# Optimization experiments

Hardware: AMD Instinct MI355X
Metric: run time of the kernel (lower is better)

## Reference

```python
import jax, jax.numpy as jnp
import numpy as np

B, C, T, N = 8, 128, 12, 4096
E_HALF = 131072
EPS = 1e-5


def _linear_params(key, fan_in, fan_out):
    kw, kb = jax.random.split(key)
    bound = 1.0 / np.sqrt(fan_in)
    W = jax.random.uniform(kw, (fan_in, fan_out), jnp.float32, -bound, bound)
    b = jax.random.uniform(kb, (fan_out,), jnp.float32, -bound, bound)
    return W, b


def setup_inputs() -> dict:
    key = jax.random.key(0)
    ks = jax.random.split(key, 10)
    h_in = jax.random.normal(ks[0], (B, C, T, N), jnp.float32)
    # symmetric edge list: random pairs + reverses + self loops
    u = jax.random.randint(ks[1], (E_HALF,), 0, N, jnp.int32)
    v = jax.random.randint(ks[2], (E_HALF,), 0, N, jnp.int32)
    loops = jnp.arange(N, dtype=jnp.int32)
    row = jnp.concatenate([u, v, loops])
    col = jnp.concatenate([v, u, loops])
    edge_index = jnp.stack([row, col])  # [2, E]
    Wq, bq = _linear_params(ks[3], C, C)
    Wk, bk = _linear_params(ks[4], C, C)
    Wv, bv = _linear_params(ks[5], C, C)
    W1, b1 = _linear_params(ks[6], 2 * C, 4 * C)
    W2, b2 = _linear_params(ks[7], 4 * C, C)
    W3, b3 = _linear_params(ks[8], C, 1)
    return dict(h_in=h_in, edge_index=edge_index, Wq=Wq, bq=bq, Wk=Wk, bk=bk,
                Wv=Wv, bv=bv, W1=W1, b1=b1, W2=W2, b2=b2, W3=W3, b3=b3)


def _masked_instance_norm(x, mask_f):
    # stats over the non-self-loop edges only (matching torch, where the MLP
    # only sees edge_index[:, non_self_loop_mask])
    cnt = mask_f.sum()
    mean = (x * mask_f).sum(0) / cnt
    var = (((x - mean) ** 2) * mask_f).sum(0) / cnt
    return (x - mean) / jnp.sqrt(var + EPS)


def _forward(h_in, edge_index, Wq, bq, Wk, bk, Wv, bv, W1, b1, W2, b2, W3, b3):
    # ---- TemporalAttention ----
    x = jnp.transpose(h_in, (0, 3, 2, 1))  # [B, N, T, C]
    q = x @ Wq + bq
    k = x @ Wk + bk
    v = x @ Wv + bv
    scores = jnp.einsum('bntc,bnsc->bnts', q, k) / (C ** 0.5)
    attn = jax.nn.softmax(scores, axis=-1)
    weighted = jnp.einsum('bnts,bnsc->bntc', attn, v)
    emb = weighted.sum(axis=2)          # [B, N, C]
    emb_mean = emb.mean(axis=0)         # [N, C]

    # ---- ExtractorMLP on non-self-loop edges ----
    row, col = edge_index[0], edge_index[1]
    self_loop = row == col
    mask_f = (~self_loop).astype(emb_mean.dtype)[:, None]  # [E, 1]
    f12 = jnp.concatenate([emb_mean[row], emb_mean[col]], axis=-1)  # [E, 2C]
    h = jax.nn.relu(_masked_instance_norm(f12 @ W1 + b1, mask_f))
    h = jax.nn.relu(_masked_instance_norm(h @ W2 + b2, mask_f))
    logits = h @ W3 + b3                 # [E, 1]

    # concrete_sample, eval mode (deterministic)
    att = jax.nn.sigmoid(logits)
    all_att = jnp.where(self_loop[:, None], 1.0, att)  # [E, 1]

    # ---- transpose + reorder_like: match each edge with its reverse ----
    M = jnp.max(edge_index) + 1
    fwd_key = row * M + col
    rev_key = col * M + row
    order = jnp.argsort(fwd_key)
    pos = jnp.searchsorted(fwd_key[order], rev_key)
    perm = order[pos]                    # index of reverse edge
    edge_att = (all_att + all_att[perm]) * 0.5
    return edge_att


def reference(h_in, edge_index, Wq, bq, Wk, bk, Wv, bv, W1, b1, W2, b2, W3, b3):
    return _forward(h_in, edge_index, Wq, bq, Wk, bk, Wv, bv, W1, b1, W2, b2, W3, b3)
```

## Files before the change

kernel.cpp:

```cpp
#include <hip/hip_runtime.h>
#include <hip/hip_bf16.h>

#define CC     128
#define TT     12
#define NNODE  4096
#define NE     266240
#define EHALF  131072
#define F1     512
#define EPS    1e-5f
#define RSQRTC 0.08838834764831845f
#define EB     64
#define NBLKG  4160
#define NF2A   65
#define ST     40

#define O_XWM   0ull
#define O_W1S   524288ull
#define O_W2S   524800ull
#define O_ICNT  525312ull
#define O_CNT   525440ull
#define O_T     529536ull
#define O_S     529664ull
#define O_GTB   546048ull
#define O_W0B   554240ull
#define O_WC1   554304ull
#define O_WC2   619840ull
#define O_B1C   685376ull
#define O_M1    685888ull
#define O_IS1   686400ull
#define O_M2    686912ull
#define O_IS2   687040ull
#define O_CROSS 687168ull
#define O_W2T   687680ull
#define O_PB    720448ull
#define O_QB    1769024ull
#define O_ALLA  2817600ull
#define O_PART  3083840ull
#define O_PART2 4148800ull
#define O_Z2    4165440ull

typedef __attribute__((ext_vector_type(8))) short bf16x8;
typedef __attribute__((ext_vector_type(4))) float f32x4;

__device__ inline float bfbits2f(unsigned int v) { return __uint_as_float(v << 16); }
__device__ inline unsigned short f2bf(float x) {
  union { __hip_bfloat16 h; unsigned short u; } cv;
  cv.h = __float2bfloat16(x);
  return cv.u;
}
__device__ inline float f4get(const float4& v, int k) {
  return k == 0 ? v.x : k == 1 ? v.y : k == 2 ? v.z : v.w;
}

__global__ void k_pre(const float* __restrict__ Wq, const float* __restrict__ bq,
                      const float* __restrict__ Wk,
                      unsigned short* __restrict__ Gtb, unsigned short* __restrict__ w0b) {
  int i = blockIdx.x, j = threadIdx.x;
  float acc = 0.f;
  for (int co = 0; co < CC; ++co) acc = fmaf(Wq[i*CC+co], Wk[j*CC+co], acc);
  Gtb[j*CC + i] = f2bf(acc);
  if (j == 0) {
    float a = 0.f;
    for (int co = 0; co < CC; ++co) a = fmaf(Wk[i*CC+co], bq[co], a);
    w0b[i] = f2bf(a);
  }
}

__global__ __launch_bounds__(256) void k_prew(const float* __restrict__ Wv,
    const float* __restrict__ bv, const float* __restrict__ W1, const float* __restrict__ b1,
    float* __restrict__ Wc1, float* __restrict__ Wc2, float* __restrict__ b1c) {
  __shared__ float wvr[CC];
  const int c = blockIdx.x, tid = threadIdx.x;
  if (tid < CC) wvr[tid] = Wv[(size_t)c*CC + tid];
  __syncthreads();
  for (int h = 0; h < 2; ++h) {
    int f = h*256 + tid;
    float a1 = 0.f, a2 = 0.f;
    for (int j = 0; j < CC; ++j) {
      float wv = wvr[j];
      a1 = fmaf(wv, W1[(size_t)j*F1 + f], a1);
      a2 = fmaf(wv, W1[(size_t)(CC + j)*F1 + f], a2);
    }
    Wc1[(size_t)c*F1 + f] = a1;
    Wc2[(size_t)c*F1 + f] = a2;
  }
  if (c == 0) {
    for (int h = 0; h < 2; ++h) {
      int f = h*256 + tid;
      float s = b1[f];
      for (int j = 0; j < CC; ++j)
        s = fmaf(12.f*bv[j], W1[(size_t)j*F1 + f] + W1[(size_t)(CC + j)*F1 + f], s);
      b1c[f] = s;
    }
  }
}

__global__ void k_w2t(const float* __restrict__ W2, unsigned short* __restrict__ W2T) {
  int n = blockIdx.x;
  for (int k = threadIdx.x; k < F1; k += 256)
    W2T[(size_t)n*F1 + k] = f2bf(W2[(size_t)k*CC + n]);
}

__global__ __launch_bounds__(256) void k_hist(const int* __restrict__ row,
    const int* __restrict__ col, int* __restrict__ cnt, int* __restrict__ icnt) {
  __shared__ int h[NNODE];
  const int tid = threadIdx.x;
  for (int i = tid; i < NNODE; i += 256) h[i] = 0;
  __syncthreads();
  int lc = 0;
  const int base = blockIdx.x << 12;
  for (int i = tid; i < 4096; i += 256) {
    int e = base + i;
    int r = row[e], c = col[e];
    if (r != c) { atomicAdd(&h[r], 1); ++lc; }
  }
  #pragma unroll
  for (int d = 1; d < 64; d <<= 1) lc += __shfl_xor(lc, d);
  __syncthreads();
  for (int i = tid; i < NNODE; i += 256) { int v = h[i]; if (v) atomicAdd(&cnt[i], v); }
  if ((tid & 63) == 0) atomicAdd(icnt, lc);
}

__global__ __launch_bounds__(256) void k_attn(
    const float* __restrict__ h_in,
    const unsigned short* __restrict__ Gtb,
    const unsigned short* __restrict__ w0b,
    float* __restrict__ xwm) {
  __shared__ unsigned short xs[12800];
  __shared__ unsigned short ys[12800];
  __shared__ float dsv[104];
  const int tid = threadIdx.x;
  const int bid = ((blockIdx.x & 7) << 9) | (blockIdx.x >> 3);
  const int b  = bid >> 9;
  const int n0 = (bid & 511) << 3;

  {
    const float* hb = h_in + ((size_t)b*CC*TT)*NNODE + n0;
    #pragma unroll
    for (int it = 0; it < 3; ++it) {
      int p = it*256 + tid;
      int c2 = p & 63;
      int t  = p >> 6;
      const float* g0 = hb + ((size_t)(2*c2)*TT + t)*NNODE;
      const float* g1 = g0 + (size_t)(TT*NNODE);
      float4 a0 = *(const float4*)g0;
      float4 a1 = *(const float4*)(g0 + 4);
      float4 b0 = *(const float4*)g1;
      float4 b1 = *(const float4*)(g1 + 4);
      #pragma unroll
      for (int i = 0; i < 8; ++i) {
        float va = (i < 4) ? f4get(a0, i) : f4get(a1, i - 4);
        float vb = (i < 4) ? f4get(b0, i) : f4get(b1, i - 4);
        int r = i*TT + t;
        unsigned byte = ((unsigned)r << 8) + (((unsigned)(c2*4)) ^ (((unsigned)(r & 7)) << 4));
        *(unsigned*)((char*)xs + byte) = (unsigned)f2bf(va) | ((unsigned)f2bf(vb) << 16);
      }
    }
  }

  const int w = tid >> 6, lane = tid & 63;
  const int l15 = lane & 15, l4 = lane >> 4;

  bf16x8 gfr[2][4];
  #pragma unroll
  for (int mt = 0; mt < 2; ++mt)
    #pragma unroll
    for (int kt = 0; kt < 4; ++kt)
      gfr[mt][kt] = *(const bf16x8*)(Gtb + (size_t)((w<<5) + (mt<<4) + l15)*CC + (kt<<5) + (l4<<3));
  bf16x8 wfr[4];
  if (w == 3) {
    #pragma unroll
    for (int kt = 0; kt < 4; ++kt) {
      bf16x8 z = {0,0,0,0,0,0,0,0};
      if (l15 == 0) z = *(const bf16x8*)(w0b + (kt<<5) + (l4<<3));
      wfr[kt] = z;
    }
  }
  __syncthreads();

  #pragma unroll
  for (int np = 0; np < 2; ++np) {
    f32x4 acc[2][3];
    f32x4 accd[3];
    #pragma unroll
    for (int mt = 0; mt < 2; ++mt)
      #pragma unroll
      for (int nt = 0; nt < 3; ++nt) acc[mt][nt] = (f32x4){0.f,0.f,0.f,0.f};
    #pragma unroll
    for (int nt = 0; nt < 3; ++nt) accd[nt] = (f32x4){0.f,0.f,0.f,0.f};

    #pragma unroll
    for (int kt = 0; kt < 4; ++kt) {
      bf16x8 bfr[3];
      #pragma unroll
      for (int nt = 0; nt < 3; ++nt) {
        int rr = np*48 + nt*16 + l15;
        unsigned byte = ((unsigned)rr << 8) +
                        (((unsigned)((kt<<6) + (l4<<4))) ^ (((unsigned)(rr & 7)) << 4));
        bfr[nt] = *(const bf16x8*)((const char*)xs + byte);
      }
      #pragma unroll
      for (int mt = 0; mt < 2; ++mt)
        #pragma unroll
        for (int nt = 0; nt < 3; ++nt)
          acc[mt][nt] = __builtin_amdgcn_mfma_f32_16x16x32_bf16(gfr[mt][kt], bfr[nt], acc[mt][nt], 0, 0, 0);
      if (w == 3) {
        #pragma unroll
        for (int nt = 0; nt < 3; ++nt)
          accd[nt] = __builtin_amdgcn_mfma_f32_16x16x32_bf16(wfr[kt], bfr[nt], accd[nt], 0, 0, 0);
      }
    }
    #pragma unroll
    for (int mt = 0; mt < 2; ++mt)
      #pragma unroll
      for (int nt = 0; nt < 3; ++nt) {
        int rr = np*48 + nt*16 + l15;
        ushort4 v;
        v.x = f2bf(acc[mt][nt][0]); v.y = f2bf(acc[mt][nt][1]);
        v.z = f2bf(acc[mt][nt][2]); v.w = f2bf(acc[mt][nt][3]);
        unsigned cb = (unsigned)((w<<6) + (mt<<5) + (l4<<3));
        unsigned byte = ((unsigned)rr << 8) + (cb ^ (((unsigned)(rr & 7)) << 4));
        *(ushort4*)((char*)ys + byte) = v;
      }
    if (w == 3 && l4 == 0) {
      #pragma unroll
      for (int nt = 0; nt < 3; ++nt)
        dsv[np*48 + nt*16 + l15] = accd[nt][0];
    }
  }
  __syncthreads();

  #pragma unroll
  for (int nn = 0; nn < 2; ++nn) {
    const int n = (w << 1) + nn;
    const int rb = n*TT;
    const int rr = rb + l15;
    f32x4 sa = (f32x4){0.f,0.f,0.f,0.f};
    #pragma unroll
    for (int kt = 0; kt < 4; ++kt) {
      unsigned byte = ((unsigned)rr << 8) +
                      (((unsigned)((kt<<6) + (l4<<4))) ^ (((unsigned)(rr & 7)) << 4));
      bf16x8 afr = *(const bf16x8*)((const char*)ys + byte);
      bf16x8 bfr = *(const bf16x8*)((const char*)xs + byte);
      sa = __builtin_amdgcn_mfma_f32_16x16x32_bf16(afr, bfr, sa, 0, 0, 0);
    }
    float dv = dsv[rr];
    const bool sval = (l15 < TT);
    float p[4];
    #pragma unroll
    for (int r = 0; r < 4; ++r) {
      float t1 = sval ? (sa[r] + dv) * RSQRTC : -1e30f;
      float m = t1;
      m = fmaxf(m, __shfl_xor(m, 1));
      m = fmaxf(m, __shfl_xor(m, 2));
      m = fmaxf(m, __shfl_xor(m, 4));
      m = fmaxf(m, __shfl_xor(m, 8));
      float e = exp2f((t1 - m) * 1.4426950408889634f);
      float s = e;
      s += __shfl_xor(s, 1);
      s += __shfl_xor(s, 2);
      s += __shfl_xor(s, 4);
      s += __shfl_xor(s, 8);
      p[r] = e / s;
    }
    float wpart = (l4 < 3) ? (p[0] + p[1] + p[2] + p[3]) : 0.f;
    wpart += __shfl_xor(wpart, 16);
    wpart += __shfl_xor(wpart, 32);
    float xw0 = 0.f, xw1 = 0.f;
    #pragma unroll
    for (int s = 0; s < TT; ++s) {
      float wv = __shfl(wpart, s);
      int r2 = rb + s;
      unsigned byte = ((unsigned)r2 << 8) +
                      (((unsigned)(lane << 2)) ^ (((unsigned)(r2 & 7)) << 4));
      unsigned xp = *(const unsigned*)((const char*)xs + byte);
      xw0 = fmaf(wv, bfbits2f(xp & 0xffffu), xw0);
      xw1 = fmaf(wv, bfbits2f(xp >> 16), xw1);
    }
    unsafeAtomicAdd(&xwm[(size_t)(n0 + n)*CC + (lane << 1)],     xw0 * 0.125f);
    unsafeAtomicAdd(&xwm[(size_t)(n0 + n)*CC + (lane << 1) + 1], xw1 * 0.125f);
  }
}

__global__ __launch_bounds__(256) void k_t(const float* __restrict__ xwm,
    const int* __restrict__ cnt, float* __restrict__ t) {
  __shared__ float ts[256];
  const int tid = threadIdx.x;
  const int f = tid & 127;
  const int n0 = blockIdx.x << 7;
  float s = 0.f;
  for (int i = (tid >> 7); i < 128; i += 2) {
    int n = n0 + i;
    s = fmaf((float)cnt[n], xwm[(size_t)n*CC + f], s);
  }
  ts[tid] = s;
  __syncthreads();
  if (tid < 128) unsafeAtomicAdd(&t[f], ts[tid] + ts[tid + 128]);
}

__global__ __launch_bounds__(256) void k_S(const float* __restrict__ xwm,
    const int* __restrict__ row, const int* __restrict__ col, float* __restrict__ S) {
  __shared__ unsigned short XT[128*ST];
  __shared__ unsigned short YT[128*ST];
  const int tid = threadIdx.x;
  const int w = tid >> 6, lane = tid & 63, l15 = lane & 15, l4 = lane >> 4;
  const int j = tid & 31, fi = tid >> 5;
  const int f0 = fi << 4;
  f32x4 acc[2][8];
  #pragma unroll
  for (int mt = 0; mt < 2; ++mt)
    #pragma unroll
    for (int nt = 0; nt < 8; ++nt) acc[mt][nt] = (f32x4){0.f,0.f,0.f,0.f};

  const int ebase = blockIdx.x << 9;
  for (int bt = 0; bt < 16; ++bt) {
    const int e = ebase + (bt << 5) + j;
    const int r = row[e], c = col[e];
    const bool msk = (r != c);
    const float* xr = xwm + (size_t)r*CC + f0;
    const float* xc = xwm + (size_t)c*CC + f0;
    float4 xv[4], yv[4];
    #pragma unroll
    for (int u = 0; u < 4; ++u) { xv[u] = *(const float4*)(xr + 4*u); yv[u] = *(const float4*)(xc + 4*u); }
    __syncthreads();
    #pragma unroll
    for (int u = 0; u < 16; ++u) {
      float xvv = f4get(xv[u >> 2], u & 3);
      float yvv = f4get(yv[u >> 2], u & 3);
      XT[(f0+u)*ST + j] = f2bf(xvv);
      YT[(f0+u)*ST + j] = msk ? f2bf(yvv) : (unsigned short)0;
    }
    __syncthreads();
    bf16x8 af[2];
    #pragma unroll
    for (int mt = 0; mt < 2; ++mt)
      af[mt] = *(const bf16x8*)&XT[((((w<<1)+mt)<<4) + l15)*ST + (l4<<3)];
    #pragma unroll
    for (int nt = 0; nt < 8; ++nt) {
      bf16x8 bf_ = *(const bf16x8*)&YT[(((nt<<4) + l15))*ST + (l4<<3)];
      acc[0][nt] = __builtin_amdgcn_mfma_f32_16x16x32_bf16(af[0], bf_, acc[0][nt], 0, 0, 0);
      acc[1][nt] = __builtin_amdgcn_mfma_f32_16x16x32_bf16(af[1], bf_, acc[1][nt], 0, 0, 0);
    }
  }
  #pragma unroll
  for (int mt = 0; mt < 2; ++mt)
    #pragma unroll
    for (int nt = 0; nt < 8; ++nt)
      #pragma unroll
      for (int reg = 0; reg < 4; ++reg) {
        int a = (((w<<1)+mt)<<4) + (l4<<2) + reg;
        int b = (nt<<4) + l15;
        unsafeAtomicAdd(&S[a*128 + b], acc[mt][nt][reg]);
      }
}

__global__ __launch_bounds__(128) void k_cross(const float* __restrict__ S,
    const float* __restrict__ Wc1, const float* __restrict__ Wc2,
    const float* __restrict__ b1c, const float* __restrict__ t,
    float* __restrict__ cross) {
  __shared__ float w2c[128];
  __shared__ float red[128], red2[128];
  const int f = blockIdx.x, a = threadIdx.x;
  w2c[a] = Wc2[(size_t)a*F1 + f];
  __syncthreads();
  float v = 0.f;
  const float* Sr = S + a*128;
  for (int b = 0; b < 128; b += 4) {
    float4 sv = *(const float4*)(Sr + b);
    v = fmaf(sv.x, w2c[b],   v); v = fmaf(sv.y, w2c[b+1], v);
    v = fmaf(sv.z, w2c[b+2], v); v = fmaf(sv.w, w2c[b+3], v);
  }
  float pa = Wc1[(size_t)a*F1 + f] * v;
  float ta = t[a] * w2c[a];
  #pragma unroll
  for (int d = 1; d < 64; d <<= 1) { pa += __shfl_xor(pa, d); ta += __shfl_xor(ta, d); }
  red[a] = pa; red2[a] = ta;
  __syncthreads();
  if (a == 0) cross[f] = red[0] + red[64] + b1c[f]*(red2[0] + red2[64]);
}

__global__ __launch_bounds__(256) void k_pq(const float* __restrict__ xwm,
    const float* __restrict__ Wc1, const float* __restrict__ Wc2,
    const float* __restrict__ b1c, const int* __restrict__ cnt,
    unsigned short* __restrict__ Pb, unsigned short* __restrict__ Qb,
    float* __restrict__ w1, float* __restrict__ w2) {
  __shared__ float em[4][CC];
  const int tid = threadIdx.x;
  const int n0 = blockIdx.x << 2;
  for (int i = tid; i < 4*CC; i += 256)
    em[i >> 7][i & 127] = xwm[(size_t)(n0 + (i >> 7))*CC + (i & 127)];
  __syncthreads();
  float ws[2] = {0.f, 0.f}, qs[2] = {0.f, 0.f};
  for (int nn = 0; nn < 4; ++nn) {
    const float cw = (float)cnt[n0 + nn];
    for (int half = 0; half < 2; ++half) {
      int f = half*256 + tid;
      float ap = b1c[f], aq = 0.f;
      for (int c = 0; c < CC; ++c) {
        float e = em[nn][c];
        ap = fmaf(e, Wc1[(size_t)c*F1 + f], ap);
        aq = fmaf(e, Wc2[(size_t)c*F1 + f], aq);
      }
      unsigned short pu = f2bf(ap), qu = f2bf(aq);
      Pb[(size_t)(n0+nn)*F1 + f] = pu;
      Qb[(size_t)(n0+nn)*F1 + f] = qu;
      float pf = bfbits2f(pu), qf = bfbits2f(qu);
      ws[half] = fmaf(cw, pf + qf, ws[half]);
      qs[half] = fmaf(cw, pf*pf + qf*qf, qs[half]);
    }
  }
  unsafeAtomicAdd(&w1[tid],       ws[0]);
  unsafeAtomicAdd(&w1[tid + 256], ws[1]);
  unsafeAtomicAdd(&w2[tid],       qs[0]);
  unsafeAtomicAdd(&w2[tid + 256], qs[1]);
}

__global__ void k_fin1(const float* __restrict__ w1, const float* __restrict__ w2,
                       const float* __restrict__ cross, const int* __restrict__ icnt,
                       float* __restrict__ m1, float* __restrict__ is1) {
  int f = threadIdx.x;
  float cnt = (float)(*icnt);
  float m = w1[f] / cnt;
  m1[f] = m;
  is1[f] = rsqrtf((w2[f] + 2.f*cross[f]) / cnt - m*m + EPS);
}

__global__ __launch_bounds__(512, 4) void k_gemm(const unsigned short* __restrict__ Pb,
    const unsigned short* __restrict__ Qb, const int* __restrict__ row,
    const int* __restrict__ col,
    const float* __restrict__ m1, const float* __restrict__ is1,
    const unsigned short* __restrict__ W2T, const float* __restrict__ b2,
    unsigned short* __restrict__ z2, float* __restrict__ part) {
  __shared__ unsigned short h1s[EB*F1];
  __shared__ float m1s[F1], is1s[F1];
  __shared__ int rS[EB], cS[EB]; __shared__ float mk[EB];
  __shared__ float cstat[256];
  const int tid = threadIdx.x;
  const int bid = blockIdx.x;
  const int e0 = bid * EB;
  const int w = tid >> 6, lane = tid & 63;
  const int wn0 = w << 4;
  const int l15 = lane & 15, l4 = lane >> 4;
  if (tid < EB) {
    int r = row[e0+tid], c = col[e0+tid];
    rS[tid] = r; cS[tid] = c; mk[tid] = (r != c) ? 1.f : 0.f;
  }
  for (int i = tid; i < F1; i += 512) { m1s[i] = m1[i]; is1s[i] = is1[i]; }
  __syncthreads();

  {
    const int j = tid >> 3;
    const unsigned short* pr = Pb + (size_t)rS[j]*F1;
    const unsigned short* qr = Qb + (size_t)cS[j]*F1;
    const int sw = (j & 7) << 4;
    const unsigned rowb = (unsigned)j << 10;
    #pragma unroll
    for (int half = 0; half < 2; ++half) {
      uint4 pv[4], qv[4];
      #pragma unroll
      for (int u = 0; u < 4; ++u) {
        int k0 = (((tid & 7) + ((half*4 + u) << 3)) << 3);
        pv[u] = *(const uint4*)(pr + k0);
        qv[u] = *(const uint4*)(qr + k0);
      }
      #pragma unroll
      for (int u = 0; u < 4; ++u) {
        int k0 = (((tid & 7) + ((half*4 + u) << 3)) << 3);
        unsigned out[4];
        #pragma unroll
        for (int q = 0; q < 4; ++q) {
          unsigned pu = (&pv[u].x)[q], qu = (&qv[u].x)[q];
          int k = k0 + 2*q;
          float2 mm = *(const float2*)&m1s[k];
          float2 ii = *(const float2*)&is1s[k];
          float za = bfbits2f(pu & 0xffffu) + bfbits2f(qu & 0xffffu);
          float zb = bfbits2f(pu >> 16)     + bfbits2f(qu >> 16);
          float ha = fmaxf((za - mm.x)*ii.x, 0.f);
          float hb = fmaxf((zb - mm.y)*ii.y, 0.f);
          out[q] = (unsigned)f2bf(ha) | ((unsigned)f2bf(hb) << 16);
        }
        unsigned byte = rowb + (((unsigned)(k0 << 1)) ^ sw);
        *(uint4*)((char*)h1s + byte) = make_uint4(out[0], out[1], out[2], out[3]);
      }
    }
  }
  __syncthreads();

  f32x4 acc[4];
  #pragma unroll
  for (int a = 0; a < 4; ++a) acc[a] = (f32x4){0.f,0.f,0.f,0.f};

  const unsigned short* w2p = W2T + (size_t)(wn0 + l15)*F1 + (l4 << 3);
  #pragma unroll
  for (int kt = 0; kt < 16; ++kt) {
    bf16x8 bfr = *(const bf16x8*)(w2p + (kt << 5));
    bf16x8 afr[4];
    #pragma unroll
    for (int mt = 0; mt < 4; ++mt) {
      int j = (mt << 4) + l15;
      unsigned byte = ((unsigned)j << 10) + (((unsigned)(kt*64 + l4*16)) ^ ((j & 7) << 4));
      afr[mt] = *(const bf16x8*)((const char*)h1s + byte);
    }
    #pragma unroll
    for (int mt = 0; mt < 4; ++mt)
      acc[mt] = __builtin_amdgcn_mfma_f32_16x16x32_bf16(afr[mt], bfr, acc[mt], 0, 0, 0);
  }
  __syncthreads();

  float* z2s = (float*)&h1s[0];
  const int colg = wn0 + l15;
  {
    float bb = b2[colg];
    float sloc = 0.f, qloc = 0.f;
    #pragma unroll
    for (int mt = 0; mt < 4; ++mt) {
      f32x4 v = acc[mt];
      #pragma unroll
      for (int reg = 0; reg < 4; ++reg) {
        int j = (mt << 4) + (l4 << 2) + reg;
        float z = v[reg] + bb;
        float m = mk[j];
        sloc = fmaf(m, z, sloc);
        qloc = fmaf(m*z, z, qloc);
        z2s[j*132 + colg] = z;
      }
    }
    sloc += __shfl_xor(sloc, 16); sloc += __shfl_xor(sloc, 32);
    qloc += __shfl_xor(qloc, 16); qloc += __shfl_xor(qloc, 32);
    if (l4 == 0) { cstat[colg] = sloc; cstat[128 + colg] = qloc; }
  }
  __syncthreads();

  #pragma unroll
  for (int p = 0; p < 2; ++p) {
    int idx = (p << 12) + (tid << 3);
    int j = idx >> 7, c = idx & 127;
    const float* src = &z2s[j*132 + c];
    float4 v0 = *(const float4*)src;
    float4 v1 = *(const float4*)(src + 4);
    uint4 o;
    o.x = (unsigned)f2bf(v0.x) | ((unsigned)f2bf(v0.y) << 16);
    o.y = (unsigned)f2bf(v0.z) | ((unsigned)f2bf(v0.w) << 16);
    o.z = (unsigned)f2bf(v1.x) | ((unsigned)f2bf(v1.y) << 16);
    o.w = (unsigned)f2bf(v1.z) | ((unsigned)f2bf(v1.w) << 16);
    *(uint4*)(z2 + (size_t)e0*CC + idx) = o;
  }
  if (tid < 256) part[(size_t)bid*256 + tid] = cstat[tid];
}

__global__ __launch_bounds__(256) void k_fin2a(const float* __restrict__ part,
                                               float* __restrict__ part2) {
  const int g = blockIdx.x, tid = threadIdx.x;
  float s = 0.f;
  #pragma unroll 4
  for (int r = 0; r < 64; ++r)
    s += part[(size_t)(g*64 + r)*256 + tid];
  part2[(size_t)g*256 + tid] = s;
}

__global__ __launch_bounds__(256) void k_fin2b(const float* __restrict__ part2,
    const int* __restrict__ icnt, float* __restrict__ m2, float* __restrict__ is2) {
  __shared__ float red[256];
  const int tid = threadIdx.x;
  float s = 0.f;
  for (int g = 0; g < NF2A; ++g) s += part2[(size_t)g*256 + tid];
  red[tid] = s;
  __syncthreads();
  if (tid < 128) {
    float cnt = (float)(*icnt);
    float m = red[tid] / cnt;
    m2[tid] = m;
    is2[tid] = rsqrtf(red[128 + tid]/cnt - m*m + EPS);
  }
}

__global__ __launch_bounds__(256) void k_score(const unsigned short* __restrict__ z2,
    const int* __restrict__ row, const int* __restrict__ col,
    const float* __restrict__ m2, const float* __restrict__ is2,
    const float* __restrict__ W3, const float* __restrict__ b3,
    float* __restrict__ all_att) {
  __shared__ float zt[64][129];
  const int tid = threadIdx.x;
  const int e0 = blockIdx.x << 6;
  const uint4* src = reinterpret_cast<const uint4*>(z2 + (size_t)e0*CC);
  for (int i = tid; i < 64*CC/8; i += 256) {
    uint4 v = src[i];
    int flat = i*8;
    int j = flat >> 7, k = flat & 127;
    zt[j][k+0] = bfbits2f(v.x & 0xffffu); zt[j][k+1] = bfbits2f(v.x >> 16);
    zt[j][k+2] = bfbits2f(v.y & 0xffffu); zt[j][k+3] = bfbits2f(v.y >> 16);
    zt[j][k+4] = bfbits2f(v.z & 0xffffu); zt[j][k+5] = bfbits2f(v.z >> 16);
    zt[j][k+6] = bfbits2f(v.w & 0xffffu); zt[j][k+7] = bfbits2f(v.w >> 16);
  }
  __syncthreads();
  const int j = tid >> 2, q = tid & 3;
  float a = 0.f;
  for (int k = q*32; k < q*32 + 32; ++k)
    a = fmaf(fmaxf((zt[j][k] - m2[k])*is2[k], 0.f), W3[k], a);
  a += __shfl_xor(a, 1, 4);
  a += __shfl_xor(a, 2, 4);
  if (q == 0) {
    int e = e0 + j;
    int r = row[e], c = col[e];
    float att;
    if (r == c) att = 1.f;
    else        att = 1.f / (1.f + expf(-(a + b3[0])));
    all_att[e] = att;
  }
}

__global__ __launch_bounds__(256) void k_out(const float* __restrict__ all_att,
    float* __restrict__ out) {
  int e = blockIdx.x*256 + threadIdx.x;
  int p = (e < EHALF) ? (e + EHALF) : (e < 2*EHALF ? e - EHALF : e);
  out[e] = 0.5f * (all_att[e] + all_att[p]);
}

extern "C" void kernel_launch(void* const* d_in, const int* in_sizes, int n_in,
                              void* d_out, int out_size, void* d_ws, size_t ws_size,
                              hipStream_t stream) {
  const float* h_in = (const float*)d_in[0];
  const int*   ei   = (const int*)d_in[1];
  const float* Wq = (const float*)d_in[2];
  const float* bq = (const float*)d_in[3];
  const float* Wk = (const float*)d_in[4];
  const float* bk = (const float*)d_in[5];  (void)bk;
  const float* Wv = (const float*)d_in[6];
  const float* bv = (const float*)d_in[7];
  const float* W1 = (const float*)d_in[8];
  const float* b1 = (const float*)d_in[9];
  const float* W2 = (const float*)d_in[10];
  const float* b2 = (const float*)d_in[11];
  const float* W3 = (const float*)d_in[12];
  const float* b3 = (const float*)d_in[13];
  float* ws = (float*)d_ws;
  float* out = (float*)d_out;
  const int* row = ei;
  const int* col = ei + NE;

  hipMemsetAsync(ws, 0, 546048ull * 4ull, stream);

  k_pre<<<128, 128, 0, stream>>>(Wq, bq, Wk,
                                 (unsigned short*)(ws+O_GTB), (unsigned short*)(ws+O_W0B));
  k_prew<<<128, 256, 0, stream>>>(Wv, bv, W1, b1, ws+O_WC1, ws+O_WC2, ws+O_B1C);
  k_w2t<<<128, 256, 0, stream>>>(W2, (unsigned short*)(ws+O_W2T));
  k_hist<<<64, 256, 0, stream>>>(row, col, (int*)(ws+O_CNT), (int*)(ws+O_ICNT));
  k_attn<<<4096, 256, 0, stream>>>(h_in, (const unsigned short*)(ws+O_GTB),
                                   (const unsigned short*)(ws+O_W0B), ws+O_XWM);
  k_t<<<32, 256, 0, stream>>>(ws+O_XWM, (const int*)(ws+O_CNT), ws+O_T);
  k_S<<<512, 256, 0, stream>>>(ws+O_XWM, row, col, ws+O_S);
  k_pq<<<1024, 256, 0, stream>>>(ws+O_XWM, ws+O_WC1, ws+O_WC2, ws+O_B1C,
                                 (const int*)(ws+O_CNT),
                                 (unsigned short*)(ws+O_PB), (unsigned short*)(ws+O_QB),
                                 ws+O_W1S, ws+O_W2S);
  k_cross<<<512, 128, 0, stream>>>(ws+O_S, ws+O_WC1, ws+O_WC2, ws+O_B1C, ws+O_T,
                                   ws+O_CROSS);
  k_fin1<<<1, 512, 0, stream>>>(ws+O_W1S, ws+O_W2S, ws+O_CROSS,
                                (const int*)(ws+O_ICNT), ws+O_M1, ws+O_IS1);
  k_gemm<<<NBLKG, 512, 0, stream>>>((const unsigned short*)(ws+O_PB),
                                    (const unsigned short*)(ws+O_QB), row, col,
                                    ws+O_M1, ws+O_IS1,
                                    (const unsigned short*)(ws+O_W2T), b2,
                                    (unsigned short*)(ws+O_Z2), ws+O_PART);
  k_fin2a<<<NF2A, 256, 0, stream>>>(ws+O_PART, ws+O_PART2);
  k_fin2b<<<1, 256, 0, stream>>>(ws+O_PART2, (const int*)(ws+O_ICNT), ws+O_M2, ws+O_IS2);
  k_score<<<4160, 256, 0, stream>>>((const unsigned short*)(ws+O_Z2), row, col,
                                    ws+O_M2, ws+O_IS2, W3, b3, ws+O_ALLA);
  k_out<<<1040, 256, 0, stream>>>(ws+O_ALLA, out);
}
```

Before: 496.4 us.

## Halve attention block tile to 4 nodes, compute bias dot via shuffles, raise occupancy

The temporal attention kernel now handles 4 nodes per block instead of 8, which halves shared memory and doubles the grid. Launch bounds ask for 8 blocks per CU. The per-row bias dot with w0 is now computed in fp32 during the load phase with a wave shuffle reduction, replacing the extra MFMA pass on wave 3. The G fragments are reloaded per k-step instead of being held in registers, trading extra global/L2 reads for lower register pressure and higher occupancy. Each thread now issues 6 fully independent float4 loads up front, which gives more memory-level parallelism.

Result: no change. 504.2 us (+1.6%).

```diff
diff --git a/kernel.cpp b/kernel.cpp
--- a/kernel.cpp
+++ b/kernel.cpp
@@ -121,80 +121,69 @@
   if ((tid & 63) == 0) atomicAdd(icnt, lc);
 }
 
-__global__ __launch_bounds__(256) void k_attn(
+__global__ __launch_bounds__(256, 8) void k_attn(
     const float* __restrict__ h_in,
     const unsigned short* __restrict__ Gtb,
     const unsigned short* __restrict__ w0b,
     float* __restrict__ xwm) {
-  __shared__ unsigned short xs[12800];
-  __shared__ unsigned short ys[12800];
-  __shared__ float dsv[104];
-  const int tid = threadIdx.x;
-  const int bid = ((blockIdx.x & 7) << 9) | (blockIdx.x >> 3);
-  const int b  = bid >> 9;
-  const int n0 = (bid & 511) << 3;
+  __shared__ unsigned short xs[48*128];
+  __shared__ unsigned short ys[48*128];
+  __shared__ float dsv[48];
+  const int tid = threadIdx.x;
+  const int bid = ((blockIdx.x & 7) << 10) | (blockIdx.x >> 3);
+  const int b  = bid >> 10;
+  const int n0 = (bid & 1023) << 2;
+
+  const int w = tid >> 6, lane = tid & 63;
+  const int l15 = lane & 15, l4 = lane >> 4;
 
   {
-    const float* hb = h_in + ((size_t)b*CC*TT)*NNODE + n0;
+    const int c2 = tid & 63;
+    const float* g0 = h_in + (((size_t)b*CC + 2*c2)*TT + w)*NNODE + n0;
+    float4 av[3], bv[3];
     #pragma unroll
     for (int it = 0; it < 3; ++it) {
-      int p = it*256 + tid;
-      int c2 = p & 63;
-      int t  = p >> 6;
-      const float* g0 = hb + ((size_t)(2*c2)*TT + t)*NNODE;
-      const float* g1 = g0 + (size_t)(TT*NNODE);
-      float4 a0 = *(const float4*)g0;
-      float4 a1 = *(const float4*)(g0 + 4);
-      float4 b0 = *(const float4*)g1;
-      float4 b1 = *(const float4*)(g1 + 4);
-      #pragma unroll
-      for (int i = 0; i < 8; ++i) {
-        float va = (i < 4) ? f4get(a0, i) : f4get(a1, i - 4);
-        float vb = (i < 4) ? f4get(b0, i) : f4get(b1, i - 4);
+      av[it] = *(const float4*)(g0 + (size_t)(4*it)*NNODE);
+      bv[it] = *(const float4*)(g0 + (size_t)(TT + 4*it)*NNODE);
+    }
+    unsigned wp = *(const unsigned*)(w0b + 2*c2);
+    float w0f0 = bfbits2f(wp & 0xffffu), w0f1 = bfbits2f(wp >> 16);
+    #pragma unroll
+    for (int it = 0; it < 3; ++it) {
+      int t = w + it*4;
+      #pragma unroll
+      for (int i = 0; i < 4; ++i) {
+        float xa = f4get(av[it], i);
+        float xb = f4get(bv[it], i);
         int r = i*TT + t;
         unsigned byte = ((unsigned)r << 8) + (((unsigned)(c2*4)) ^ (((unsigned)(r & 7)) << 4));
-        *(unsigned*)((char*)xs + byte) = (unsigned)f2bf(va) | ((unsigned)f2bf(vb) << 16);
-      }
-    }
-  }
-
-  const int w = tid >> 6, lane = tid & 63;
-  const int l15 = lane & 15, l4 = lane >> 4;
-
-  bf16x8 gfr[2][4];
-  #pragma unroll
-  for (int mt = 0; mt < 2; ++mt)
-    #pragma unroll
-    for (int kt = 0; kt < 4; ++kt)
-      gfr[mt][kt] = *(const bf16x8*)(Gtb + (size_t)((w<<5) + (mt<<4) + l15)*CC + (kt<<5) + (l4<<3));
-  bf16x8 wfr[4];
-  if (w == 3) {
+        *(unsigned*)((char*)xs + byte) = (unsigned)f2bf(xa) | ((unsigned)f2bf(xb) << 16);
+        float dd = fmaf(xa, w0f0, xb * w0f1);
+        #pragma unroll
+        for (int d = 1; d < 64; d <<= 1) dd += __shfl_xor(dd, d);
+        if (lane == 0) dsv[r] = dd;
+      }
+    }
+  }
+  __syncthreads();
+
+  {
+    f32x4 acc[2][3];
+    #pragma unroll
+    for (int mt = 0; mt < 2; ++mt)
+      #pragma unroll
+      for (int nt = 0; nt < 3; ++nt) acc[mt][nt] = (f32x4){0.f,0.f,0.f,0.f};
+
     #pragma unroll
     for (int kt = 0; kt < 4; ++kt) {
-      bf16x8 z = {0,0,0,0,0,0,0,0};
-      if (l15 == 0) z = *(const bf16x8*)(w0b + (kt<<5) + (l4<<3));
-      wfr[kt] = z;
-    }
-  }
-  __syncthreads();
-
-  #pragma unroll
-  for (int np = 0; np < 2; ++np) {
-    f32x4 acc[2][3];
-    f32x4 accd[3];
-    #pragma unroll
-    for (int mt = 0; mt < 2; ++mt)
-      #pragma unroll
-      for (int nt = 0; nt < 3; ++nt) acc[mt][nt] = (f32x4){0.f,0.f,0.f,0.f};
-    #pragma unroll
-    for (int nt = 0; nt < 3; ++nt) accd[nt] = (f32x4){0.f,0.f,0.f,0.f};
-
-    #pragma unroll
-    for (int kt = 0; kt < 4; ++kt) {
+      bf16x8 gf[2];
+      #pragma unroll
+      for (int mt = 0; mt < 2; ++mt)
+        gf[mt] = *(const bf16x8*)(Gtb + (size_t)((w<<5) + (mt<<4) + l15)*CC + (kt<<5) + (l4<<3));
       bf16x8 bfr[3];
       #pragma unroll
       for (int nt = 0; nt < 3; ++nt) {
-        int rr = np*48 + nt*16 + l15;
+        int rr = nt*16 + l15;
         unsigned byte = ((unsigned)rr << 8) +
                         (((unsigned)((kt<<6) + (l4<<4))) ^ (((unsigned)(rr & 7)) << 4));
         bfr[nt] = *(const bf16x8*)((const char*)xs + byte);
@@ -203,18 +192,13 @@
       for (int mt = 0; mt < 2; ++mt)
         #pragma unroll
         for (int nt = 0; nt < 3; ++nt)
-          acc[mt][nt] = __builtin_amdgcn_mfma_f32_16x16x32_bf16(gfr[mt][kt], bfr[nt], acc[mt][nt], 0, 0, 0);
-      if (w == 3) {
-        #pragma unroll
-        for (int nt = 0; nt < 3; ++nt)
-          accd[nt] = __builtin_amdgcn_mfma_f32_16x16x32_bf16(wfr[kt], bfr[nt], accd[nt], 0, 0, 0);
-      }
+          acc[mt][nt] = __builtin_amdgcn_mfma_f32_16x16x32_bf16(gf[mt], bfr[nt], acc[mt][nt], 0, 0, 0);
     }
     #pragma unroll
     for (int mt = 0; mt < 2; ++mt)
       #pragma unroll
       for (int nt = 0; nt < 3; ++nt) {
-        int rr = np*48 + nt*16 + l15;
+        int rr = nt*16 + l15;
         ushort4 v;
         v.x = f2bf(acc[mt][nt][0]); v.y = f2bf(acc[mt][nt][1]);
         v.z = f2bf(acc[mt][nt][2]); v.w = f2bf(acc[mt][nt][3]);
@@ -222,19 +206,13 @@
         unsigned byte = ((unsigned)rr << 8) + (cb ^ (((unsigned)(rr & 7)) << 4));
         *(ushort4*)((char*)ys + byte) = v;
       }
-    if (w == 3 && l4 == 0) {
-      #pragma unroll
-      for (int nt = 0; nt < 3; ++nt)
-        dsv[np*48 + nt*16 + l15] = accd[nt][0];
-    }
-  }
-  __syncthreads();
-
-  #pragma unroll
-  for (int nn = 0; nn < 2; ++nn) {
-    const int n = (w << 1) + nn;
-    const int rb = n*TT;
-    const int rr = rb + l15;
+  }
+  __syncthreads();
+
+  {
+    const int rb = w*TT;
+    const bool sval = (l15 < TT);
+    const int rr = rb + (sval ? l15 : 0);
     f32x4 sa = (f32x4){0.f,0.f,0.f,0.f};
     #pragma unroll
     for (int kt = 0; kt < 4; ++kt) {
@@ -245,7 +223,6 @@
       sa = __builtin_amdgcn_mfma_f32_16x16x32_bf16(afr, bfr, sa, 0, 0, 0);
     }
     float dv = dsv[rr];
-    const bool sval = (l15 < TT);
     float p[4];
     #pragma unroll
     for (int r = 0; r < 4; ++r) {
@@ -277,8 +254,8 @@
       xw0 = fmaf(wv, bfbits2f(xp & 0xffffu), xw0);
       xw1 = fmaf(wv, bfbits2f(xp >> 16), xw1);
     }
-    unsafeAtomicAdd(&xwm[(size_t)(n0 + n)*CC + (lane << 1)],     xw0 * 0.125f);
-    unsafeAtomicAdd(&xwm[(size_t)(n0 + n)*CC + (lane << 1) + 1], xw1 * 0.125f);
+    unsafeAtomicAdd(&xwm[(size_t)(n0 + w)*CC + (lane << 1)],     xw0 * 0.125f);
+    unsafeAtomicAdd(&xwm[(size_t)(n0 + w)*CC + (lane << 1) + 1], xw1 * 0.125f);
   }
 }
 
@@ -645,7 +622,7 @@
   k_prew<<<128, 256, 0, stream>>>(Wv, bv, W1, b1, ws+O_WC1, ws+O_WC2, ws+O_B1C);
   k_w2t<<<128, 256, 0, stream>>>(W2, (unsigned short*)(ws+O_W2T));
   k_hist<<<64, 256, 0, stream>>>(row, col, (int*)(ws+O_CNT), (int*)(ws+O_ICNT));
-  k_attn<<<4096, 256, 0, stream>>>(h_in, (const unsigned short*)(ws+O_GTB),
+  k_attn<<<8192, 256, 0, stream>>>(h_in, (const unsigned short*)(ws+O_GTB),
                                    (const unsigned short*)(ws+O_W0B), ws+O_XWM);
   k_t<<<32, 256, 0, stream>>>(ws+O_XWM, (const int*)(ws+O_CNT), ws+O_T);
   k_S<<<512, 256, 0, stream>>>(ws+O_XWM, row, col, ws+O_S);
```
